# Performance work log

Hardware: AMD Instinct MI355X
Metric: run time of the kernel (lower is better)

## Reference

```python
import jax, jax.numpy as jnp
import numpy as np

B, RES, DIM, H, KD = 16, 32, 768, 12, 64
N = RES * RES          # 1024 tokens
D = KD                 # attn_ratio = 1 -> per-head value dim == key_dim
DH = D * H             # 768
SCALE = KD ** -0.5
LN_EPS = 1e-5


def _bias_idxs():
    # replicate the itertools.product construction: for row-major points,
    # offsets (|dy|,|dx|) are first seen in order dy-major, so id = |dy|*RES + |dx|
    coords = np.arange(N)
    y, x = coords // RES, coords % RES
    dy = np.abs(y[:, None] - y[None, :])
    dx = np.abs(x[:, None] - x[None, :])
    return jnp.asarray(dy * RES + dx, dtype=jnp.int32)  # [N, N]


def setup_inputs() -> dict:
    key = jax.random.key(0)
    ks = jax.random.split(key, 8)
    return {
        "x": jax.random.normal(ks[0], (B, N, DIM), jnp.float32),
        "ln_w": 1.0 + 0.01 * jax.random.normal(ks[1], (DIM,), jnp.float32),
        "ln_b": 0.01 * jax.random.normal(ks[2], (DIM,), jnp.float32),
        "qkv_w": 0.02 * jax.random.normal(ks[3], (3 * H * KD, DIM), jnp.float32),
        "qkv_b": 0.01 * jax.random.normal(ks[4], (3 * H * KD,), jnp.float32),
        "proj_w": 0.02 * jax.random.normal(ks[5], (DIM, DH), jnp.float32),
        "proj_b": 0.01 * jax.random.normal(ks[6], (DIM,), jnp.float32),
        "attn_biases": 0.1 * jax.random.normal(ks[7], (H, RES * RES), jnp.float32),
        "bias_idxs": _bias_idxs(),
    }


def reference(x, ln_w, ln_b, qkv_w, qkv_b, proj_w, proj_b, attn_biases, bias_idxs):
    # LayerNorm over the feature dim
    mu = jnp.mean(x, axis=-1, keepdims=True)
    var = jnp.mean(jnp.square(x - mu), axis=-1, keepdims=True)
    xn = (x - mu) * jax.lax.rsqrt(var + LN_EPS) * ln_w + ln_b

    # fused qkv projection -> [B, N, H, 3*KD], split per head
    qkv = (xn @ qkv_w.T + qkv_b).reshape(B, N, H, 3 * KD)
    q, k, v = jnp.split(qkv, [KD, 2 * KD], axis=3)  # each [B, N, H, KD]

    # gathered relative-position bias: [H, N, N]
    bias = attn_biases[:, bias_idxs]

    # scores + bias -> softmax -> AV
    attn = jnp.einsum("bnhk,bmhk->bhnm", q, k) * SCALE + bias[None]
    attn = jax.nn.softmax(attn, axis=-1)
    out = jnp.einsum("bhnm,bmhd->bnhd", attn, v).reshape(B, N, DH)
    return out @ proj_w.T + proj_b
```

## Files before the change

kernel.cpp:

```cpp
#include <hip/hip_runtime.h>
#include <cstdint>
#include <cstddef>

#define AS1 __attribute__((address_space(1)))
#define AS3 __attribute__((address_space(3)))

typedef float f32x4 __attribute__((ext_vector_type(4)));
typedef __bf16 bf16x8 __attribute__((ext_vector_type(8)));
typedef __bf16 bf16x4 __attribute__((ext_vector_type(4)));
typedef _Float16 h16x4 __attribute__((ext_vector_type(4)));
typedef uint32_t u32x4 __attribute__((ext_vector_type(4)));

__device__ __forceinline__ void async_cp16(void* lds, const void* g) {
    __builtin_amdgcn_global_load_lds((AS1 void*)(g), (AS3 void*)(lds), 16, 0, 0);
}

__device__ __forceinline__ bf16x8 frag_of(u32x4 u) {
    return __builtin_bit_cast(bf16x8, u);
}

__global__ __launch_bounds__(256)
void cvt_w(const float* __restrict__ qkvw, const float* __restrict__ projw,
           __bf16* __restrict__ qkvwb, __bf16* __restrict__ projwb) {
    int i = blockIdx.x * 256 + threadIdx.x;
    if (i < 442368) {
        int row = i / 192, c4 = (i - row * 192) * 4;
        int t = (row >= 1536) ? 2 : (row >= 768 ? 1 : 0);
        int rem = row - t * 768;
        int hh = rem >> 6, d = rem & 63;
        int in_row = hh * 192 + t * 64 + d;
        float4 v = *(const float4*)(qkvw + (long)in_row * 768 + c4);
        bf16x4 o;
        o[0] = (__bf16)v.x; o[1] = (__bf16)v.y; o[2] = (__bf16)v.z; o[3] = (__bf16)v.w;
        *(bf16x4*)(qkvwb + (long)row * 768 + c4) = o;
    } else {
        int j = i - 442368;
        float4 v = ((const float4*)projw)[j];
        bf16x4 o;
        o[0] = (__bf16)v.x; o[1] = (__bf16)v.y; o[2] = (__bf16)v.z; o[3] = (__bf16)v.w;
        ((bf16x4*)projwb)[j] = o;
    }
}

__global__ __launch_bounds__(256)
void ln_kernel(const float* __restrict__ x, const float* __restrict__ w,
               const float* __restrict__ bsh, __bf16* __restrict__ xn) {
    const int lane = threadIdx.x & 63;
    const long row = (long)blockIdx.x * 4 + (threadIdx.x >> 6);
    const float4* xr = (const float4*)(x + row * 768);
    float4 v[3];
    v[0] = xr[lane]; v[1] = xr[lane + 64]; v[2] = xr[lane + 128];
    float s = 0.f, ss = 0.f;
#pragma unroll
    for (int i = 0; i < 3; ++i) {
        s  += v[i].x + v[i].y + v[i].z + v[i].w;
        ss += v[i].x * v[i].x + v[i].y * v[i].y + v[i].z * v[i].z + v[i].w * v[i].w;
    }
#pragma unroll
    for (int m = 1; m < 64; m <<= 1) { s += __shfl_xor(s, m); ss += __shfl_xor(ss, m); }
    const float mean = s * (1.f / 768.f);
    const float rstd = rsqrtf(ss * (1.f / 768.f) - mean * mean + 1e-5f);
    const float4* wv = (const float4*)w;
    const float4* bv = (const float4*)bsh;
    bf16x4* outp = (bf16x4*)(xn + row * 768);
#pragma unroll
    for (int i = 0; i < 3; ++i) {
        float4 wi = wv[lane + 64 * i], bi = bv[lane + 64 * i];
        bf16x4 o;
        o[0] = (__bf16)((v[i].x - mean) * rstd * wi.x + bi.x);
        o[1] = (__bf16)((v[i].y - mean) * rstd * wi.y + bi.y);
        o[2] = (__bf16)((v[i].z - mean) * rstd * wi.z + bi.z);
        o[3] = (__bf16)((v[i].w - mean) * rstd * wi.w + bi.w);
        outp[lane + 64 * i] = o;
    }
}

template <int MODE>
__device__ __forceinline__
void gemm_core(__bf16* As, __bf16* Bs,
               const __bf16* __restrict__ A, const __bf16* __restrict__ Bw,
               const float* __restrict__ bias,
               __bf16* __restrict__ q_out, __bf16* __restrict__ k_out,
               __bf16* __restrict__ vt_out, float* __restrict__ f_out,
               long bm, long bn) {
    constexpr int K = 768;
    const int tid  = threadIdx.x;
    const int lane = tid & 63;
    const int quad = lane >> 4;
    const int l16  = lane & 15;
    const int wave = tid >> 6;
    const int wm = wave >> 1, wn = wave & 1;

    const __bf16* Ab = A  + bm * K;
    const __bf16* Bb = Bw + bn * K;

    const int el0 = tid, el1 = tid + 256;
    const int rA0 = el0 >> 2, rA1 = el1 >> 2;
    const int kc  = (tid & 3) * 8;

    f32x4 acc[4][4] = {};

    for (int k0 = 0; k0 < K; k0 += 32) {
        __syncthreads();
        async_cp16((char*)As + el0 * 16, Ab + (long)rA0 * K + (k0 + kc));
        async_cp16((char*)As + el1 * 16, Ab + (long)rA1 * K + (k0 + kc));
        async_cp16((char*)Bs + el0 * 16, Bb + (long)rA0 * K + (k0 + kc));
        async_cp16((char*)Bs + el1 * 16, Bb + (long)rA1 * K + (k0 + kc));
        __syncthreads();

        const u32x4* Av = (const u32x4*)As;
        const u32x4* Bv = (const u32x4*)Bs;
        bf16x8 af[4], bfr[4];
#pragma unroll
        for (int t = 0; t < 4; ++t) {
            af[t]  = frag_of(Av[(wm * 64 + t * 16 + l16) * 4 + quad]);
            bfr[t] = frag_of(Bv[(wn * 64 + t * 16 + l16) * 4 + quad]);
        }
#pragma unroll
        for (int i = 0; i < 4; ++i)
#pragma unroll
            for (int j = 0; j < 4; ++j) {
                if constexpr (MODE == 0)
                    acc[i][j] = __builtin_amdgcn_mfma_f32_16x16x32_bf16(bfr[j], af[i], acc[i][j], 0, 0, 0);
                else
                    acc[i][j] = __builtin_amdgcn_mfma_f32_16x16x32_bf16(af[i], bfr[j], acc[i][j], 0, 0, 0);
            }
    }

    if constexpr (MODE == 0) {
#pragma unroll
        for (int j = 0; j < 4; ++j) {
            int col0 = (int)bn + wn * 64 + j * 16 + quad * 4;
            int t  = col0 >= 768;
            int cc = col0 - t * 768;
            int h  = cc >> 6, d = cc & 63;
            int f  = h * 192 + t * 64 + d;
            float4 bb = *(const float4*)(bias + f);
            __bf16* dst = t ? k_out : q_out;
#pragma unroll
            for (int i = 0; i < 4; ++i) {
                long row = bm + wm * 64 + i * 16 + l16;
                long b   = row >> 10;
                long n   = row & 1023;
                bf16x4 pk;
                pk[0] = (__bf16)(acc[i][j][0] + bb.x);
                pk[1] = (__bf16)(acc[i][j][1] + bb.y);
                pk[2] = (__bf16)(acc[i][j][2] + bb.z);
                pk[3] = (__bf16)(acc[i][j][3] + bb.w);
                *(bf16x4*)(dst + ((b * 12 + h) * 1024 + n) * 64 + d) = pk;
            }
        }
    } else if constexpr (MODE == 2) {
#pragma unroll
        for (int j = 0; j < 4; ++j) {
            int cv = (int)bn - 1536 + wn * 64 + j * 16 + l16;
            int h  = cv >> 6, d = cv & 63;
            float bv = bias[h * 192 + 128 + d];
#pragma unroll
            for (int i = 0; i < 4; ++i) {
                long row0 = bm + wm * 64 + i * 16 + quad * 4;
                long b    = row0 >> 10;
                long n0   = row0 & 1023;
                bf16x4 pk;
                pk[0] = (__bf16)(acc[i][j][0] + bv);
                pk[1] = (__bf16)(acc[i][j][1] + bv);
                pk[2] = (__bf16)(acc[i][j][2] + bv);
                pk[3] = (__bf16)(acc[i][j][3] + bv);
                *(bf16x4*)(vt_out + ((b * 12 + h) * 64 + d) * 1024 + n0) = pk;
            }
        }
    } else {
#pragma unroll
        for (int i = 0; i < 4; ++i) {
#pragma unroll
            for (int r = 0; r < 4; ++r) {
                long row = bm + wm * 64 + i * 16 + quad * 4 + r;
#pragma unroll
                for (int j = 0; j < 4; ++j) {
                    int col = (int)bn + wn * 64 + j * 16 + l16;
                    f_out[row * 768 + col] = acc[i][j][r] + bias[col];
                }
            }
        }
    }
}

__global__ __launch_bounds__(256, 3)
void gemm_qkv(const __bf16* __restrict__ A, const __bf16* __restrict__ Bw,
              const float* __restrict__ bias, __bf16* __restrict__ qb,
              __bf16* __restrict__ kb, __bf16* __restrict__ vtb) {
    __shared__ __align__(16) __bf16 As[128 * 32];
    __shared__ __align__(16) __bf16 Bs[128 * 32];
    int blk  = blockIdx.x;
    int xcd  = blk & 7;
    int rest = blk >> 3;
    int bx   = rest % 18;
    int byg  = rest / 18;
    long by  = xcd + 8 * byg;
    if (bx < 12)
        gemm_core<0>(As, Bs, A, Bw, bias, qb, kb, nullptr, nullptr, by * 128, (long)bx * 128);
    else
        gemm_core<2>(As, Bs, A, Bw, bias, nullptr, nullptr, vtb, nullptr, by * 128, (long)bx * 128);
}

__global__ __launch_bounds__(256, 3)
void gemm_proj(const __bf16* __restrict__ A, const __bf16* __restrict__ Bw,
               const float* __restrict__ bias, float* __restrict__ out) {
    __shared__ __align__(16) __bf16 As[128 * 32];
    __shared__ __align__(16) __bf16 Bs[128 * 32];
    int blk  = blockIdx.x;
    int xcd  = blk & 7;
    int rest = blk >> 3;
    int bx   = rest % 6;
    int byg  = rest / 6;
    long by  = xcd + 8 * byg;
    gemm_core<1>(As, Bs, A, Bw, bias, nullptr, nullptr, nullptr, out,
                 by * 128, (long)bx * 128);
}

__global__ __launch_bounds__(256, 6)
void attn_kernel(const __bf16* __restrict__ Q, const __bf16* __restrict__ Kb,
                 const __bf16* __restrict__ Vt, const float* __restrict__ biases,
                 __bf16* __restrict__ out) {
    __shared__ __align__(16) __bf16 QPs[64 * 64];
    __shared__ __align__(16) __bf16 Ks[64 * 64];
    __shared__ __align__(16) __bf16 Vts[64 * 64];
    __shared__ __align__(16) _Float16 brow[1024];

    const int tid  = threadIdx.x;
    const int lane = tid & 63;
    const int wave = tid >> 6;
    const int quad = lane >> 4;
    const int l16  = lane & 15;
    const int sw   = l16 & 7;

    int blk  = blockIdx.x;
    int xcd  = blk & 7;
    int rest = blk >> 3;
    int qt   = rest & 15;
    int bhg  = rest >> 4;
    int bh_i = xcd + 8 * bhg;
    int b    = bh_i / 12;
    int h    = bh_i - b * 12;

    const long bh = bh_i;
    const __bf16* Qg  = Q  + (bh * 1024 + qt * 64) * 64;
    const __bf16* Kg  = Kb + bh * 1024 * 64;
    const __bf16* Vtg = Vt + bh * 64 * 1024;

    const int e0 = tid, e1 = tid + 256;
    const int r0 = e0 >> 3, c0 = (e0 & 7) ^ (r0 & 7);
    const int r1 = e1 >> 3, c1 = (e1 & 7) ^ (r1 & 7);

    async_cp16((char*)QPs + e0 * 16, Qg + r0 * 64 + c0 * 8);
    async_cp16((char*)QPs + e1 * 16, Qg + r1 * 64 + c1 * 8);
    {
        const float LOG2E = 1.4426950408889634f;
        float4 v = ((const float4*)(biases + (long)h * 1024))[tid];
        h16x4 o;
        o[0] = (_Float16)(v.x * LOG2E); o[1] = (_Float16)(v.y * LOG2E);
        o[2] = (_Float16)(v.z * LOG2E); o[3] = (_Float16)(v.w * LOG2E);
        *(h16x4*)(brow + tid * 4) = o;
    }
    __syncthreads();

    bf16x8 aq[2];
    {
        const u32x4* Qv = (const u32x4*)QPs;
        int qrow = wave * 16 + l16;
        aq[0] = frag_of(Qv[qrow * 8 + (quad ^ sw)]);
        aq[1] = frag_of(Qv[qrow * 8 + ((quad + 4) ^ sw)]);
    }

    const int yq = 2 * qt + (wave >> 1);
    const int xq = ((wave & 1) << 4) + l16;
    int pdx[2][4];
#pragma unroll
    for (int i2 = 0; i2 < 2; ++i2)
#pragma unroll
        for (int r = 0; r < 4; ++r) {
            int xk = (i2 << 4) + quad * 4 + r;
            int d = xq - xk; pdx[i2][r] = d < 0 ? -d : d;
        }

    const float SSCALE = 0.125f * 1.4426950408889634f;
    float lacc = 0.f;
    f32x4 o[4] = {};
    __bf16* Psw = QPs + wave * 1024;
    const int pwb = l16 * 128 + (quad & 1) * 8;

    for (int kt = 0; kt < 16; ++kt) {
        __syncthreads();
        {
            const __bf16* Kt  = Kg + kt * 4096;
            const __bf16* Vtt = Vtg + kt * 64;
            async_cp16((char*)Ks + e0 * 16, Kt + r0 * 64 + c0 * 8);
            async_cp16((char*)Ks + e1 * 16, Kt + r1 * 64 + c1 * 8);
            async_cp16((char*)Vts + e0 * 16, Vtt + r0 * 1024 + c0 * 8);
            async_cp16((char*)Vts + e1 * 16, Vtt + r1 * 1024 + c1 * 8);
        }
        __syncthreads();

        f32x4 s[4];
        const u32x4* Kv = (const u32x4*)Ks;
#pragma unroll
        for (int nt = 0; nt < 4; ++nt) {
            int krow = nt * 16 + l16;
            bf16x8 k0 = frag_of(Kv[krow * 8 + (quad ^ sw)]);
            bf16x8 k1 = frag_of(Kv[krow * 8 + ((quad + 4) ^ sw)]);
            f32x4 z = {0.f, 0.f, 0.f, 0.f};
            z = __builtin_amdgcn_mfma_f32_16x16x32_bf16(k0, aq[0], z, 0, 0, 0);
            z = __builtin_amdgcn_mfma_f32_16x16x32_bf16(k1, aq[1], z, 0, 0, 0);
            s[nt] = z;
        }

        int dy0 = yq - 2 * kt;     dy0 = dy0 < 0 ? -dy0 : dy0;
        int dy1 = yq - 2 * kt - 1; dy1 = dy1 < 0 ? -dy1 : dy1;
        const _Float16* br0 = brow + dy0 * 32;
        const _Float16* br1 = brow + dy1 * 32;
#pragma unroll
        for (int nt = 0; nt < 4; ++nt) {
            const _Float16* br = (nt & 2) ? br1 : br0;
            bf16x4 pk;
#pragma unroll
            for (int r = 0; r < 4; ++r) {
                float p = __builtin_amdgcn_exp2f(s[nt][r] * SSCALE + (float)br[pdx[nt & 1][r]]);
                lacc += p;
                pk[r] = (__bf16)p;
            }
            *(bf16x4*)((char*)Psw + pwb + (((nt * 2 + (quad >> 1)) ^ sw) << 4)) = pk;
        }

        const u32x4* Pv = (const u32x4*)Psw;
        const u32x4* Vv = (const u32x4*)Vts;
        bf16x8 bp0 = frag_of(Pv[l16 * 8 + (quad ^ sw)]);
        bf16x8 bp1 = frag_of(Pv[l16 * 8 + ((quad + 4) ^ sw)]);
#pragma unroll
        for (int dt = 0; dt < 4; ++dt) {
            int vrow = dt * 16 + l16;
            bf16x8 v0 = frag_of(Vv[vrow * 8 + (quad ^ sw)]);
            bf16x8 v1 = frag_of(Vv[vrow * 8 + ((quad + 4) ^ sw)]);
            o[dt] = __builtin_amdgcn_mfma_f32_16x16x32_bf16(v0, bp0, o[dt], 0, 0, 0);
            o[dt] = __builtin_amdgcn_mfma_f32_16x16x32_bf16(v1, bp1, o[dt], 0, 0, 0);
        }
    }

    lacc += __shfl_xor(lacc, 16);
    lacc += __shfl_xor(lacc, 32);
    const float rl = 1.f / lacc;

    const long n = qt * 64 + wave * 16 + l16;
    __bf16* op = out + ((long)b * 1024 + n) * 768 + h * 64 + quad * 4;
#pragma unroll
    for (int dt = 0; dt < 4; ++dt) {
        bf16x4 ov;
        ov[0] = (__bf16)(o[dt][0] * rl);
        ov[1] = (__bf16)(o[dt][1] * rl);
        ov[2] = (__bf16)(o[dt][2] * rl);
        ov[3] = (__bf16)(o[dt][3] * rl);
        *(bf16x4*)(op + dt * 16) = ov;
    }
}

extern "C" void kernel_launch(void* const* d_in, const int* in_sizes, int n_in,
                              void* d_out, int out_size, void* d_ws, size_t ws_size,
                              hipStream_t stream) {
    (void)in_sizes; (void)n_in; (void)out_size; (void)ws_size;
    const float* x      = (const float*)d_in[0];
    const float* ln_w   = (const float*)d_in[1];
    const float* ln_b   = (const float*)d_in[2];
    const float* qkv_w  = (const float*)d_in[3];
    const float* qkv_b  = (const float*)d_in[4];
    const float* proj_w = (const float*)d_in[5];
    const float* proj_b = (const float*)d_in[6];
    const float* ab     = (const float*)d_in[7];
    float* outp = (float*)d_out;

    char* ws = (char*)d_ws;
    __bf16* xn     = (__bf16*)(ws);
    __bf16* aout   = (__bf16*)(ws);
    __bf16* qkvwb  = (__bf16*)(ws + 25165824);
    __bf16* projwb = (__bf16*)(ws + 28704768);
    __bf16* qb     = (__bf16*)(ws + 29884416);
    __bf16* kb     = (__bf16*)(ws + 55050240);
    __bf16* vtb    = (__bf16*)(ws + 80216064);

    cvt_w<<<2304, 256, 0, stream>>>(qkv_w, proj_w, qkvwb, projwb);
    ln_kernel<<<4096, 256, 0, stream>>>(x, ln_w, ln_b, xn);
    gemm_qkv<<<2304, 256, 0, stream>>>(xn, qkvwb, qkv_b, qb, kb, vtb);
    attn_kernel<<<3072, 256, 0, stream>>>(qb, kb, vtb, ab, aout);
    gemm_proj<<<768, 256, 0, stream>>>(aout, projwb, proj_b, outp);
}
```

Measured before the change: 324.0 us.

## Double-buffer K/V tiles and double query rows per attention block

The attention kernel now runs 512-thread blocks that each own 128 query rows instead of 64, so every K/V tile staged in LDS is reused by twice as many waves. K and V tiles are double-buffered: the next tile's async copy is issued before computing on the current one, with one barrier per iteration instead of two. The relative-position bias row is now kept in LDS as fp32 rather than fp16, which removes a conversion and some rounding. In exchange LDS use per block grows, so fewer blocks fit per CU. The launch-bounds minimum-occupancy hint of 6 blocks is now unreachable at 512 threads and may squeeze the register budget.

```diff
diff --git a/kernel.cpp b/kernel.cpp
--- a/kernel.cpp
+++ b/kernel.cpp
@@ -218,14 +218,14 @@
                  by * 128, (long)bx * 128);
 }
 
-__global__ __launch_bounds__(256, 6)
+__global__ __launch_bounds__(512, 6)
 void attn_kernel(const __bf16* __restrict__ Q, const __bf16* __restrict__ Kb,
                  const __bf16* __restrict__ Vt, const float* __restrict__ biases,
                  __bf16* __restrict__ out) {
-    __shared__ __align__(16) __bf16 QPs[64 * 64];
-    __shared__ __align__(16) __bf16 Ks[64 * 64];
-    __shared__ __align__(16) __bf16 Vts[64 * 64];
-    __shared__ __align__(16) _Float16 brow[1024];
+    __shared__ __align__(16) __bf16 QPs[128 * 64];
+    __shared__ __align__(16) __bf16 Ks[2][64 * 64];
+    __shared__ __align__(16) __bf16 Vts[2][64 * 64];
+    __shared__ __align__(16) float brow[1024];
 
     const int tid  = threadIdx.x;
     const int lane = tid & 63;
@@ -237,30 +237,33 @@
     int blk  = blockIdx.x;
     int xcd  = blk & 7;
     int rest = blk >> 3;
-    int qt   = rest & 15;
-    int bhg  = rest >> 4;
+    int qt   = rest & 7;
+    int bhg  = rest >> 3;
     int bh_i = xcd + 8 * bhg;
     int b    = bh_i / 12;
     int h    = bh_i - b * 12;
 
     const long bh = bh_i;
-    const __bf16* Qg  = Q  + (bh * 1024 + qt * 64) * 64;
+    const __bf16* Qg  = Q  + (bh * 1024 + qt * 128) * 64;
     const __bf16* Kg  = Kb + bh * 1024 * 64;
     const __bf16* Vtg = Vt + bh * 64 * 1024;
 
-    const int e0 = tid, e1 = tid + 256;
-    const int r0 = e0 >> 3, c0 = (e0 & 7) ^ (r0 & 7);
-    const int r1 = e1 >> 3, c1 = (e1 & 7) ^ (r1 & 7);
-
-    async_cp16((char*)QPs + e0 * 16, Qg + r0 * 64 + c0 * 8);
-    async_cp16((char*)QPs + e1 * 16, Qg + r1 * 64 + c1 * 8);
+    {
+        const int e0 = tid, e1 = tid + 512;
+        const int r0 = e0 >> 3, c0 = (e0 & 7) ^ (r0 & 7);
+        const int r1 = e1 >> 3, c1 = (e1 & 7) ^ (r1 & 7);
+        async_cp16((char*)QPs + e0 * 16, Qg + r0 * 64 + c0 * 8);
+        async_cp16((char*)QPs + e1 * 16, Qg + r1 * 64 + c1 * 8);
+    }
+    const int rk = tid >> 3;
+    const int ck = (tid & 7) ^ (rk & 7);
+    async_cp16((char*)Ks[0]  + tid * 16, Kg  + rk * 64   + ck * 8);
+    async_cp16((char*)Vts[0] + tid * 16, Vtg + rk * 1024 + ck * 8);
     {
         const float LOG2E = 1.4426950408889634f;
-        float4 v = ((const float4*)(biases + (long)h * 1024))[tid];
-        h16x4 o;
-        o[0] = (_Float16)(v.x * LOG2E); o[1] = (_Float16)(v.y * LOG2E);
-        o[2] = (_Float16)(v.z * LOG2E); o[3] = (_Float16)(v.w * LOG2E);
-        *(h16x4*)(brow + tid * 4) = o;
+        float2 v = ((const float2*)(biases + (long)h * 1024))[tid];
+        float2 o; o.x = v.x * LOG2E; o.y = v.y * LOG2E;
+        *(float2*)(brow + tid * 2) = o;
     }
     __syncthreads();
 
@@ -272,7 +275,7 @@
         aq[1] = frag_of(Qv[qrow * 8 + ((quad + 4) ^ sw)]);
     }
 
-    const int yq = 2 * qt + (wave >> 1);
+    const int yq = 4 * qt + (wave >> 1);
     const int xq = ((wave & 1) << 4) + l16;
     int pdx[2][4];
 #pragma unroll
@@ -290,19 +293,17 @@
     const int pwb = l16 * 128 + (quad & 1) * 8;
 
     for (int kt = 0; kt < 16; ++kt) {
-        __syncthreads();
-        {
-            const __bf16* Kt  = Kg + kt * 4096;
-            const __bf16* Vtt = Vtg + kt * 64;
-            async_cp16((char*)Ks + e0 * 16, Kt + r0 * 64 + c0 * 8);
-            async_cp16((char*)Ks + e1 * 16, Kt + r1 * 64 + c1 * 8);
-            async_cp16((char*)Vts + e0 * 16, Vtt + r0 * 1024 + c0 * 8);
-            async_cp16((char*)Vts + e1 * 16, Vtt + r1 * 1024 + c1 * 8);
-        }
-        __syncthreads();
+        const int cb = kt & 1;
+        if (kt < 15) {
+            const int nb = cb ^ 1;
+            const __bf16* Kt  = Kg  + (kt + 1) * 4096;
+            const __bf16* Vtt = Vtg + (kt + 1) * 64;
+            async_cp16((char*)Ks[nb]  + tid * 16, Kt  + rk * 64   + ck * 8);
+            async_cp16((char*)Vts[nb] + tid * 16, Vtt + rk * 1024 + ck * 8);
+        }
 
         f32x4 s[4];
-        const u32x4* Kv = (const u32x4*)Ks;
+        const u32x4* Kv = (const u32x4*)Ks[cb];
 #pragma unroll
         for (int nt = 0; nt < 4; ++nt) {
             int krow = nt * 16 + l16;
@@ -316,15 +317,15 @@
 
         int dy0 = yq - 2 * kt;     dy0 = dy0 < 0 ? -dy0 : dy0;
         int dy1 = yq - 2 * kt - 1; dy1 = dy1 < 0 ? -dy1 : dy1;
-        const _Float16* br0 = brow + dy0 * 32;
-        const _Float16* br1 = brow + dy1 * 32;
+        const float* br0 = brow + dy0 * 32;
+        const float* br1 = brow + dy1 * 32;
 #pragma unroll
         for (int nt = 0; nt < 4; ++nt) {
-            const _Float16* br = (nt & 2) ? br1 : br0;
+            const float* br = (nt & 2) ? br1 : br0;
             bf16x4 pk;
 #pragma unroll
             for (int r = 0; r < 4; ++r) {
-                float p = __builtin_amdgcn_exp2f(s[nt][r] * SSCALE + (float)br[pdx[nt & 1][r]]);
+                float p = __builtin_amdgcn_exp2f(s[nt][r] * SSCALE + br[pdx[nt & 1][r]]);
                 lacc += p;
                 pk[r] = (__bf16)p;
             }
@@ -332,7 +333,7 @@
         }
 
         const u32x4* Pv = (const u32x4*)Psw;
-        const u32x4* Vv = (const u32x4*)Vts;
+        const u32x4* Vv = (const u32x4*)Vts[cb];
         bf16x8 bp0 = frag_of(Pv[l16 * 8 + (quad ^ sw)]);
         bf16x8 bp1 = frag_of(Pv[l16 * 8 + ((quad + 4) ^ sw)]);
 #pragma unroll
@@ -343,13 +344,15 @@
             o[dt] = __builtin_amdgcn_mfma_f32_16x16x32_bf16(v0, bp0, o[dt], 0, 0, 0);
             o[dt] = __builtin_amdgcn_mfma_f32_16x16x32_bf16(v1, bp1, o[dt], 0, 0, 0);
         }
+
+        __syncthreads();
     }
 
     lacc += __shfl_xor(lacc, 16);
     lacc += __shfl_xor(lacc, 32);
     const float rl = 1.f / lacc;
 
-    const long n = qt * 64 + wave * 16 + l16;
+    const long n = qt * 128 + wave * 16 + l16;
     __bf16* op = out + ((long)b * 1024 + n) * 768 + h * 64 + quad * 4;
 #pragma unroll
     for (int dt = 0; dt < 4; ++dt) {
@@ -388,6 +391,6 @@
     cvt_w<<<2304, 256, 0, stream>>>(qkv_w, proj_w, qkvwb, projwb);
     ln_kernel<<<4096, 256, 0, stream>>>(x, ln_w, ln_b, xn);
     gemm_qkv<<<2304, 256, 0, stream>>>(xn, qkvwb, qkv_b, qb, kb, vtb);
-    attn_kernel<<<3072, 256, 0, stream>>>(qb, kb, vtb, ab, aout);
+    attn_kernel<<<1536, 512, 0, stream>>>(qb, kb, vtb, ab, aout);
     gemm_proj<<<768, 256, 0, stream>>>(aout, projwb, proj_b, outp);
 }
```

Measured after the change: 311.0 us. -4.0%, faster.
